# Kernel tuning notes

Measured on AMD Instinct MI355X. Metric: run time of the kernel, lower is better.

The kernel has to match this reference:

```python
import jax, jax.numpy as jnp
import numpy as np

FP8_MAX = 448.0
SCALE = 1.0  # FP8ScalingFactor init_scale; update_scale is a no-op in eval mode


def quantize_to_fp8(t, scale):
    # Faithful emulation of the torch quantize_to_fp8 elementwise chain.
    scaled = jnp.clip(t * scale, -FP8_MAX, FP8_MAX)
    exponent = jnp.floor(jnp.log2(jnp.abs(scaled) + 1e-10))
    mantissa_step = jnp.exp2(exponent - 3.0)  # e4m3-style 3 mantissa bits
    quantized = jnp.round(scaled / mantissa_step) * mantissa_step
    return quantized / scale


def setup_inputs() -> dict:
    key = jax.random.key(0)
    k1, k2, k3 = jax.random.split(key, 3)
    B, DIN, DOUT = 8192, 4096, 16384
    x = jax.random.normal(k1, (B, DIN), dtype=jnp.float32)
    # kaiming_uniform_(a=sqrt(5)) -> bound = sqrt(3 / fan_in)
    wb = float(np.sqrt(3.0 / DIN))
    weight = jax.random.uniform(k2, (DOUT, DIN), dtype=jnp.float32, minval=-wb, maxval=wb)
    bb = float(1.0 / np.sqrt(DIN))
    bias = jax.random.uniform(k3, (DOUT,), dtype=jnp.float32, minval=-bb, maxval=bb)
    return {"x": x, "weight": weight, "bias": bias}


def reference(x, weight, bias):
    s_in, s_w = SCALE, SCALE
    fp8_x = quantize_to_fp8(x, s_in)          # [B, DIN]
    fp8_w = quantize_to_fp8(weight, s_w)      # [DOUT, DIN]
    out = jnp.einsum('bi,oi->bo', fp8_x, fp8_w)  # [B, DOUT]
    out = out / (s_in * s_w)
    return out + bias
```

## Files before the change

kernel.cpp:

```cpp
#include <hip/hip_runtime.h>
#include <hip/hip_bf16.h>


typedef int i32x4 __attribute__((ext_vector_type(4)));
typedef int i32x8 __attribute__((ext_vector_type(8)));
typedef float f32x16 __attribute__((ext_vector_type(16)));

#define BM 128
#define BN 128
#define BK 128

__global__ __launch_bounds__(256) void quant8(
    const float4* __restrict__ in, int2* __restrict__ out, int n8, float scale) {
    int i = blockIdx.x * blockDim.x + threadIdx.x;
    if (i >= n8) return;
    float4 a = in[i * 2];
    float4 b = in[i * 2 + 1];
    float c0 = fminf(fmaxf(a.x, -448.f), 448.f) * scale;
    float c1 = fminf(fmaxf(a.y, -448.f), 448.f) * scale;
    float c2 = fminf(fmaxf(a.z, -448.f), 448.f) * scale;
    float c3 = fminf(fmaxf(a.w, -448.f), 448.f) * scale;
    float c4 = fminf(fmaxf(b.x, -448.f), 448.f) * scale;
    float c5 = fminf(fmaxf(b.y, -448.f), 448.f) * scale;
    float c6 = fminf(fmaxf(b.z, -448.f), 448.f) * scale;
    float c7 = fminf(fmaxf(b.w, -448.f), 448.f) * scale;
    int lo = __builtin_amdgcn_cvt_pk_fp8_f32(c0, c1, 0, false);
    lo = __builtin_amdgcn_cvt_pk_fp8_f32(c2, c3, lo, true);
    int hi = __builtin_amdgcn_cvt_pk_fp8_f32(c4, c5, 0, false);
    hi = __builtin_amdgcn_cvt_pk_fp8_f32(c6, c7, hi, true);
    out[i] = make_int2(lo, hi);
}

__device__ __forceinline__ void gload_lds16(const void* g, void* l) {
    __builtin_amdgcn_global_load_lds(
        (const __attribute__((address_space(1))) void*)g,
        (__attribute__((address_space(3))) void*)l,
        16, 0, 0);
}

__device__ __forceinline__ i32x8 frag32(const unsigned char* base, int row, int c0) {
    const int sw = (row & 7) << 4;
    const unsigned char* p = base + row * 128;
    i32x4 lo = *(const i32x4*)(p + (c0 ^ sw));
    i32x4 hi = *(const i32x4*)(p + ((c0 + 16) ^ sw));
    i32x8 r;
    r[0] = lo[0]; r[1] = lo[1]; r[2] = lo[2]; r[3] = lo[3];
    r[4] = hi[0]; r[5] = hi[1]; r[6] = hi[2]; r[7] = hi[3];
    return r;
}

__global__ __launch_bounds__(256, 2) void gemm_fp8(
    const unsigned char* __restrict__ A, const unsigned char* __restrict__ B,
    const float* __restrict__ bias, float* __restrict__ C,
    int M, int N, int K) {
    __shared__ unsigned char lA[BM * BK];
    __shared__ unsigned char lB[BN * BK];

    const int tid = threadIdx.x;
    const int lane = tid & 63;
    const int wave = tid >> 6;
    const int wr = wave >> 1;
    const int wc = wave & 1;

    const int nwg = gridDim.x;
    const int per = nwg >> 3;
    const int bid = blockIdx.x;
    const int wg = (bid & 7) * per + (bid >> 3);
    const int mtiles = M / BM;
    const int bm = wg % mtiles;
    const int bn = wg / mtiles;

    const int arow0 = bm * BM, bcol0 = bn * BN;
    const int NT = K / BK;

    const int rl = lane & 31;
    const int g2 = lane >> 5;

    const unsigned char* const Ag = A + (size_t)arow0 * K;
    const unsigned char* const Bg = B + (size_t)bcol0 * K;

    const int srow = tid >> 3;
    const int ssrc_col = ((tid & 7) * 16) ^ (((tid >> 3) & 7) << 4);
    const int sdst = tid * 16;

    f32x16 acc[2][2] = {};

    for (int t = 0; t < NT; ++t) {
        const int kt = t * BK;
#pragma unroll
        for (int i = 0; i < 4; ++i)
            gload_lds16(Ag + (size_t)(i * 32 + srow) * K + kt + ssrc_col,
                        lA + i * 4096 + sdst);
#pragma unroll
        for (int i = 0; i < 4; ++i)
            gload_lds16(Bg + (size_t)(i * 32 + srow) * K + kt + ssrc_col,
                        lB + i * 4096 + sdst);
        __syncthreads();

#pragma unroll
        for (int ks = 0; ks < 2; ++ks) {
            const int c0 = ks * 64 + g2 * 32;
            i32x8 af[2], bf[2];
#pragma unroll
            for (int m = 0; m < 2; ++m)
                af[m] = frag32(lA, wr * 64 + m * 32 + rl, c0);
#pragma unroll
            for (int n = 0; n < 2; ++n)
                bf[n] = frag32(lB, wc * 64 + n * 32 + rl, c0);
#pragma unroll
            for (int m = 0; m < 2; ++m)
#pragma unroll
                for (int n = 0; n < 2; ++n)
                    acc[m][n] = __builtin_amdgcn_mfma_scale_f32_32x32x64_f8f6f4(
                        af[m], bf[n], acc[m][n],
                        0, 0,
                        0, 0x7F7F7F7F,
                        0, 0x79797979);
        }
        __syncthreads();
    }

#pragma unroll
    for (int n = 0; n < 2; ++n) {
        int col = bcol0 + wc * 64 + n * 32 + rl;
        float bv = bias[col];
#pragma unroll
        for (int m = 0; m < 2; ++m) {
            int rowb = arow0 + wr * 64 + m * 32 + g2 * 4;
#pragma unroll
            for (int reg = 0; reg < 16; ++reg) {
                int row = rowb + (reg & 3) + 8 * (reg >> 2);
                C[(size_t)row * N + col] = acc[m][n][reg] + bv;
            }
        }
    }
}

extern "C" void kernel_launch(void* const* d_in, const int* in_sizes, int n_in,
                              void* d_out, int out_size, void* d_ws, size_t ws_size,
                              hipStream_t stream) {
    const float* x = (const float*)d_in[0];
    const float* w = (const float*)d_in[1];
    const float* bias = (const float*)d_in[2];
    float* out = (float*)d_out;

    const int N = in_sizes[2];
    const int K = in_sizes[1] / N;
    const int M = in_sizes[0] / K;

    unsigned char* xq = (unsigned char*)d_ws;
    unsigned char* wq = xq + (size_t)M * K;

    int nx8 = M * K / 8;
    int nw8 = N * K / 8;
    quant8<<<(nx8 + 255) / 256, 256, 0, stream>>>(
        (const float4*)x, (int2*)xq, nx8, 1.0f);
    quant8<<<(nw8 + 255) / 256, 256, 0, stream>>>(
        (const float4*)w, (int2*)wq, nw8, 64.0f);

    int nwg = (M / BM) * (N / BN);
    gemm_fp8<<<nwg, 256, 0, stream>>>(
        xq, wq, bias, out, M, N, K);
}
```

Measured before the change: 804.2 us.

## Enlarge FP8 GEMM tiles to 256x256 with double-buffered LDS prefetch

The GEMM workgroup tile grows from 128x128 to 256x256, with 512 threads (8 waves) and 128 KB of dynamic LDS. The LDS is split into two buffers, so the global-to-LDS loads for the next K-slice are issued before the MFMAs on the current slice and overlap with them. This also removes one barrier per iteration. Each wave now holds a 4x2 grid of 32x32 accumulators, which raises data reuse per LDS fragment load but also raises register pressure and forces one workgroup per CU.

```diff
diff --git a/kernel.cpp b/kernel.cpp
--- a/kernel.cpp
+++ b/kernel.cpp
@@ -6,8 +6,8 @@
 typedef int i32x8 __attribute__((ext_vector_type(8)));
 typedef float f32x16 __attribute__((ext_vector_type(16)));
 
-#define BM 128
-#define BN 128
+#define BM 256
+#define BN 256
 #define BK 128
 
 __global__ __launch_bounds__(256) void quant8(
@@ -49,18 +49,17 @@
     return r;
 }
 
-__global__ __launch_bounds__(256, 2) void gemm_fp8(
+__global__ __launch_bounds__(512, 1) void gemm_fp8(
     const unsigned char* __restrict__ A, const unsigned char* __restrict__ B,
     const float* __restrict__ bias, float* __restrict__ C,
     int M, int N, int K) {
-    __shared__ unsigned char lA[BM * BK];
-    __shared__ unsigned char lB[BN * BK];
+    extern __shared__ unsigned char lds[];
 
     const int tid = threadIdx.x;
     const int lane = tid & 63;
     const int wave = tid >> 6;
-    const int wr = wave >> 1;
-    const int wc = wave & 1;
+    const int wr = wave >> 2;
+    const int wc = wave & 3;
 
     const int nwg = gridDim.x;
     const int per = nwg >> 3;
@@ -83,32 +82,42 @@
     const int ssrc_col = ((tid & 7) * 16) ^ (((tid >> 3) & 7) << 4);
     const int sdst = tid * 16;
 
-    f32x16 acc[2][2] = {};
+    auto stage = [&](const unsigned char* Gp, unsigned char* Lp, int kt) {
+#pragma unroll
+        for (int c = 0; c < 4; ++c)
+            gload_lds16(Gp + (size_t)(c * 64 + srow) * K + kt + ssrc_col,
+                        Lp + c * 8192 + sdst);
+    };
+
+    f32x16 acc[4][2] = {};
+
+    stage(Ag, lds, 0);
+    stage(Bg, lds + 32768, 0);
+    __syncthreads();
 
     for (int t = 0; t < NT; ++t) {
-        const int kt = t * BK;
-#pragma unroll
-        for (int i = 0; i < 4; ++i)
-            gload_lds16(Ag + (size_t)(i * 32 + srow) * K + kt + ssrc_col,
-                        lA + i * 4096 + sdst);
-#pragma unroll
-        for (int i = 0; i < 4; ++i)
-            gload_lds16(Bg + (size_t)(i * 32 + srow) * K + kt + ssrc_col,
-                        lB + i * 4096 + sdst);
-        __syncthreads();
+        const int cur = t & 1;
+        const unsigned char* Ab = lds + cur * 65536;
+        const unsigned char* Bb = Ab + 32768;
+        unsigned char* Anx = lds + (cur ^ 1) * 65536;
+
+        if (t + 1 < NT) {
+            stage(Ag, Anx, (t + 1) * BK);
+            stage(Bg, Anx + 32768, (t + 1) * BK);
+        }
 
 #pragma unroll
         for (int ks = 0; ks < 2; ++ks) {
             const int c0 = ks * 64 + g2 * 32;
-            i32x8 af[2], bf[2];
-#pragma unroll
-            for (int m = 0; m < 2; ++m)
-                af[m] = frag32(lA, wr * 64 + m * 32 + rl, c0);
+            i32x8 af[4], bf[2];
 #pragma unroll
             for (int n = 0; n < 2; ++n)
-                bf[n] = frag32(lB, wc * 64 + n * 32 + rl, c0);
+                bf[n] = frag32(Bb, wc * 64 + n * 32 + rl, c0);
 #pragma unroll
-            for (int m = 0; m < 2; ++m)
+            for (int m = 0; m < 4; ++m)
+                af[m] = frag32(Ab, wr * 128 + m * 32 + rl, c0);
+#pragma unroll
+            for (int m = 0; m < 4; ++m)
 #pragma unroll
                 for (int n = 0; n < 2; ++n)
                     acc[m][n] = __builtin_amdgcn_mfma_scale_f32_32x32x64_f8f6f4(
@@ -117,6 +126,7 @@
                         0, 0x7F7F7F7F,
                         0, 0x79797979);
         }
+
         __syncthreads();
     }
 
@@ -125,8 +135,8 @@
         int col = bcol0 + wc * 64 + n * 32 + rl;
         float bv = bias[col];
 #pragma unroll
-        for (int m = 0; m < 2; ++m) {
-            int rowb = arow0 + wr * 64 + m * 32 + g2 * 4;
+        for (int m = 0; m < 4; ++m) {
+            int rowb = arow0 + wr * 128 + m * 32 + g2 * 4;
 #pragma unroll
             for (int reg = 0; reg < 16; ++reg) {
                 int row = rowb + (reg & 3) + 8 * (reg >> 2);
@@ -158,7 +168,10 @@
     quant8<<<(nw8 + 255) / 256, 256, 0, stream>>>(
         (const float4*)w, (int2*)wq, nw8, 64.0f);
 
+    hipFuncSetAttribute((const void*)gemm_fp8,
+                        hipFuncAttributeMaxDynamicSharedMemorySize, 131072);
+
     int nwg = (M / BM) * (N / BN);
-    gemm_fp8<<<nwg, 256, 0, stream>>>(
+    gemm_fp8<<<nwg, 512, 131072, stream>>>(
         xq, wq, bias, out, M, N, K);
 }
```

After: 795.7 us. Within noise of the previous version (-1.1%).

## Double-buffer LDS and widen GEMM tile to 128x256 with eight waves

Applied to the files above, without the earlier changes.

The GEMM now stages the next K-slice into a second LDS buffer while the current one is consumed, which removes one barrier per iteration and overlaps global loads with MFMA work. The block tile grows to 128x256 with BK shrunk to 64, launched as 512 threads (8 waves in a 2x4 layout), and the swizzle is adapted to 64-byte rows. This improves operand reuse per block and hides load latency, at the cost of more LDS per block (48KB), fewer blocks in the grid, and less MFMA work between barriers.

```diff
diff --git a/kernel.cpp b/kernel.cpp
--- a/kernel.cpp
+++ b/kernel.cpp
@@ -7,8 +7,8 @@
 typedef float f32x16 __attribute__((ext_vector_type(16)));
 
 #define BM 128
-#define BN 128
-#define BK 128
+#define BN 256
+#define BK 64
 
 __global__ __launch_bounds__(256) void quant8(
     const float4* __restrict__ in, int2* __restrict__ out, int n8, float scale) {
@@ -39,8 +39,8 @@
 }
 
 __device__ __forceinline__ i32x8 frag32(const unsigned char* base, int row, int c0) {
-    const int sw = (row & 7) << 4;
-    const unsigned char* p = base + row * 128;
+    const int sw = (row & 3) << 4;
+    const unsigned char* p = base + row * 64;
     i32x4 lo = *(const i32x4*)(p + (c0 ^ sw));
     i32x4 hi = *(const i32x4*)(p + ((c0 + 16) ^ sw));
     i32x8 r;
@@ -49,18 +49,17 @@
     return r;
 }
 
-__global__ __launch_bounds__(256, 2) void gemm_fp8(
+__global__ __launch_bounds__(512, 2) void gemm_fp8(
     const unsigned char* __restrict__ A, const unsigned char* __restrict__ B,
     const float* __restrict__ bias, float* __restrict__ C,
     int M, int N, int K) {
-    __shared__ unsigned char lA[BM * BK];
-    __shared__ unsigned char lB[BN * BK];
+    __shared__ unsigned char lds[49152];
 
     const int tid = threadIdx.x;
     const int lane = tid & 63;
     const int wave = tid >> 6;
-    const int wr = wave >> 1;
-    const int wc = wave & 1;
+    const int wr = wave >> 2;
+    const int wc = wave & 3;
 
     const int nwg = gridDim.x;
     const int per = nwg >> 3;
@@ -75,48 +74,50 @@
 
     const int rl = lane & 31;
     const int g2 = lane >> 5;
+    const int c0 = g2 * 32;
 
     const unsigned char* const Ag = A + (size_t)arow0 * K;
     const unsigned char* const Bg = B + (size_t)bcol0 * K;
 
-    const int srow = tid >> 3;
-    const int ssrc_col = ((tid & 7) * 16) ^ (((tid >> 3) & 7) << 4);
+    const int srow = tid >> 2;
+    const int scol = ((tid & 3) << 4) ^ (((tid >> 2) & 3) << 4);
     const int sdst = tid * 16;
+
+    auto stage = [&](unsigned char* Lp, int kt) {
+        gload_lds16(Ag + (size_t)srow * K + kt + scol, Lp + sdst);
+#pragma unroll
+        for (int c = 0; c < 2; ++c)
+            gload_lds16(Bg + (size_t)(c * 128 + srow) * K + kt + scol,
+                        Lp + 8192 + c * 8192 + sdst);
+    };
 
     f32x16 acc[2][2] = {};
 
+    stage(lds, 0);
+    __syncthreads();
+
     for (int t = 0; t < NT; ++t) {
-        const int kt = t * BK;
-#pragma unroll
-        for (int i = 0; i < 4; ++i)
-            gload_lds16(Ag + (size_t)(i * 32 + srow) * K + kt + ssrc_col,
-                        lA + i * 4096 + sdst);
-#pragma unroll
-        for (int i = 0; i < 4; ++i)
-            gload_lds16(Bg + (size_t)(i * 32 + srow) * K + kt + ssrc_col,
-                        lB + i * 4096 + sdst);
-        __syncthreads();
+        const int cur = t & 1;
+        const unsigned char* Ab = lds + cur * 24576;
+        const unsigned char* Bb = Ab + 8192;
+        unsigned char* Anx = lds + (cur ^ 1) * 24576;
 
-#pragma unroll
-        for (int ks = 0; ks < 2; ++ks) {
-            const int c0 = ks * 64 + g2 * 32;
-            i32x8 af[2], bf[2];
-#pragma unroll
-            for (int m = 0; m < 2; ++m)
-                af[m] = frag32(lA, wr * 64 + m * 32 + rl, c0);
-#pragma unroll
-            for (int n = 0; n < 2; ++n)
-                bf[n] = frag32(lB, wc * 64 + n * 32 + rl, c0);
-#pragma unroll
-            for (int m = 0; m < 2; ++m)
-#pragma unroll
-                for (int n = 0; n < 2; ++n)
-                    acc[m][n] = __builtin_amdgcn_mfma_scale_f32_32x32x64_f8f6f4(
-                        af[m], bf[n], acc[m][n],
-                        0, 0,
-                        0, 0x7F7F7F7F,
-                        0, 0x79797979);
-        }
+        if (t + 1 < NT) stage(Anx, (t + 1) * BK);
+
+        i32x8 bf0 = frag32(Bb, wc * 64 + rl, c0);
+        i32x8 bf1 = frag32(Bb, wc * 64 + 32 + rl, c0);
+        i32x8 af0 = frag32(Ab, wr * 64 + rl, c0);
+        i32x8 af1 = frag32(Ab, wr * 64 + 32 + rl, c0);
+
+        acc[0][0] = __builtin_amdgcn_mfma_scale_f32_32x32x64_f8f6f4(
+            af0, bf0, acc[0][0], 0, 0, 0, 0x7F7F7F7F, 0, 0x79797979);
+        acc[0][1] = __builtin_amdgcn_mfma_scale_f32_32x32x64_f8f6f4(
+            af0, bf1, acc[0][1], 0, 0, 0, 0x7F7F7F7F, 0, 0x79797979);
+        acc[1][0] = __builtin_amdgcn_mfma_scale_f32_32x32x64_f8f6f4(
+            af1, bf0, acc[1][0], 0, 0, 0, 0x7F7F7F7F, 0, 0x79797979);
+        acc[1][1] = __builtin_amdgcn_mfma_scale_f32_32x32x64_f8f6f4(
+            af1, bf1, acc[1][1], 0, 0, 0, 0x7F7F7F7F, 0, 0x79797979);
+
         __syncthreads();
     }
 
@@ -159,6 +160,6 @@
         (const float4*)w, (int2*)wq, nw8, 64.0f);
 
     int nwg = (M / BM) * (N / BN);
-    gemm_fp8<<<nwg, 256, 0, stream>>>(
+    gemm_fp8<<<nwg, 512, 0, stream>>>(
         xq, wq, bias, out, M, N, K);
 }
```

Result: no change. 794.2 us (-1.3%).
